# Kernel tuning notes

Hardware: AMD Instinct MI355X
Metric: run time of the kernel (lower is better)

## Reference

```python
import jax, jax.numpy as jnp
import numpy as np

N_NODES = 50000
N_EDGES = 500000
N_RELS = 460
D = 128
N_LAYERS = 2
RRELU_SLOPE = (1.0 / 8.0 + 1.0 / 3.0) / 2.0  # F.rrelu eval-mode negative slope


def setup_inputs() -> dict:
    key = jax.random.key(0)
    ks = jax.random.split(key, 9)
    return {
        "node_feats": jax.random.normal(ks[0], (N_NODES, D), dtype=jnp.float32),
        "rel_emb": jax.random.normal(ks[1], (N_RELS, D), dtype=jnp.float32),
        "norm": jax.random.uniform(ks[2], (N_NODES, 1), dtype=jnp.float32),
        "edge_src": jax.random.randint(ks[3], (N_EDGES,), 0, N_NODES, dtype=jnp.int32),
        "edge_dst": jax.random.randint(ks[4], (N_EDGES,), 0, N_NODES, dtype=jnp.int32),
        "edge_rel": jax.random.randint(ks[5], (N_EDGES,), 0, N_RELS, dtype=jnp.int32),
        "W_neigh": jax.random.normal(ks[6], (N_LAYERS, D, D), dtype=jnp.float32) * 0.05,
        "W_loop": jax.random.normal(ks[7], (N_LAYERS, D, D), dtype=jnp.float32) * 0.05,
        "W_evolve": jax.random.normal(ks[8], (N_LAYERS, D, D), dtype=jnp.float32) * 0.05,
    }


def reference(node_feats, rel_emb, norm, edge_src, edge_dst, edge_rel,
              W_neigh, W_loop, W_evolve):
    """RGCNCell with 2 UnionRGCNLayers (eval mode, dropout off)."""
    n = node_feats.shape[0]
    # nodes with in-degree > 0 use loop_weight, others evolve_loop_weight
    indeg = jax.ops.segment_sum(jnp.ones_like(edge_dst, dtype=node_feats.dtype),
                                edge_dst, num_segments=n)
    has_in = (indeg > 0)[:, None]  # [N,1]

    h = node_feats
    for l in range(W_neigh.shape[0]):
        # self-loop message: choose weight per node by in-degree mask
        loop_msg = jnp.where(has_in, h @ W_loop[l], h @ W_evolve[l])  # [N,D]
        # message: gather src h + relation emb, transform  (gather-GEMM)
        msg = (h[edge_src] + rel_emb[edge_rel]) @ W_neigh[l]  # [E,D]
        # scatter-sum to dst, then apply per-node norm (apply_func)
        agg = jax.ops.segment_sum(msg, edge_dst, num_segments=n) * norm  # [N,D]
        h = agg + loop_msg
        # F.rrelu in eval mode == leaky relu with slope (lower+upper)/2
        h = jnp.where(h >= 0, h, RRELU_SLOPE * h)
    return h
```

## Files before the change

### kernel.cpp

```cpp
#include <hip/hip_runtime.h>

#define DD 128
#define CAP 64
static constexpr float SLOPE = (1.0f/8.0f + 1.0f/3.0f) * 0.5f;

typedef __attribute__((ext_vector_type(8))) short bf16x8;
typedef __attribute__((ext_vector_type(4))) float f32x4;

__device__ inline unsigned short f2bf(float x) {
    unsigned u = __builtin_bit_cast(unsigned, x);
    unsigned r = (u + 0x7FFFu + ((u >> 16) & 1u)) >> 16;
    return (unsigned short)r;
}
__device__ inline float bflo(unsigned u) {
    unsigned v = u << 16; return __builtin_bit_cast(float, v);
}
__device__ inline float bfhi(unsigned u) {
    unsigned v = u & 0xFFFF0000u; return __builtin_bit_cast(float, v);
}
__device__ inline float2 bf2f2(unsigned u) {
    return make_float2(bflo(u), bfhi(u));
}

__global__ __launch_bounds__(256) void init_k(
    const float* __restrict__ Wn, const float* __restrict__ Wl,
    const float* __restrict__ node, const float* __restrict__ rel_emb,
    unsigned short* __restrict__ Wt, int* __restrict__ slots,
    unsigned short* __restrict__ hbf, int N, int R, int NB)
{
    int b = blockIdx.x;
    if (b < 64) {
        int i = b * 256 + threadIdx.x;
        int l = i >> 13;
        int rem = i & 8191;
        int n = rem >> 5;
        int k0 = (rem & 31) * 4;
        const float* src = (n < 128) ? (Wn + l * DD * DD + n)
                                     : (Wl + l * DD * DD + (n - 128));
        unsigned short o0 = f2bf(src[(k0 + 0) * DD]);
        unsigned short o1 = f2bf(src[(k0 + 1) * DD]);
        unsigned short o2 = f2bf(src[(k0 + 2) * DD]);
        unsigned short o3 = f2bf(src[(k0 + 3) * DD]);
        *(ushort4*)&Wt[((size_t)l * 256 + n) * DD + k0] = make_ushort4(o0, o1, o2, o3);
    } else if (b < 64 + NB) {
        int i = (b - 64) * 256 + threadIdx.x;
        if (i < N) slots[i] = 0;
    } else {
        long c = (long)(b - 64 - NB) * 256 + threadIdx.x;
        long total = (long)(N + R) * 16;
        if (c >= total) return;
        long r = c >> 4;
        int  ch = (int)(c & 15);
        const float* s = (r < N) ? (node + r * DD + ch * 8)
                                 : (rel_emb + (r - N) * DD + ch * 8);
        float4 v0 = *(const float4*)s;
        float4 v1 = *(const float4*)(s + 4);
        union { bf16x8 v; unsigned short u[8]; } t;
        t.u[0] = f2bf(v0.x); t.u[1] = f2bf(v0.y);
        t.u[2] = f2bf(v0.z); t.u[3] = f2bf(v0.w);
        t.u[4] = f2bf(v1.x); t.u[5] = f2bf(v1.y);
        t.u[6] = f2bf(v1.z); t.u[7] = f2bf(v1.w);
        *(bf16x8*)&hbf[r * DD + ch * 8] = t.v;
    }
}

__global__ __launch_bounds__(256) void fill_k(const int* __restrict__ esrc,
                                              const int* __restrict__ edst,
                                              const int* __restrict__ erel,
                                              int* __restrict__ slots,
                                              int* __restrict__ spack, int E) {
    int e = blockIdx.x * 256 + threadIdx.x;
    if (e >= E) return;
    int d = edst[e];
    int slot = atomicAdd(&slots[d], 1);
    if (slot < CAP) spack[(size_t)d * CAP + slot] = esrc[e] | (erel[e] << 17);
}

__global__ __launch_bounds__(512) void gemm_dual_mfma_k(
    const unsigned short* __restrict__ Abf,
    const unsigned short* __restrict__ Wt,
    unsigned short* __restrict__ hWn,
    unsigned short* __restrict__ loopm,
    unsigned short* __restrict__ rW,
    int N, int M)
{
    __shared__ unsigned short Wsm[256 * DD];
    int tid = threadIdx.x;
    int w = tid >> 6, lane = tid & 63;
    int wm = w >> 2, wn = w & 3;
    int g = lane >> 4, q = lane & 15;
    int row0 = blockIdx.x * 128 + wm * 64;

    bf16x8 a[4][4];
    #pragma unroll
    for (int s = 0; s < 4; ++s)
        #pragma unroll
        for (int mi = 0; mi < 4; ++mi) {
            int r = row0 + mi * 16 + q;
            if (r >= M) r = M - 1;
            a[s][mi] = *(const bf16x8*)&Abf[(size_t)r * DD + s * 32 + g * 8];
        }

    #pragma unroll
    for (int it = 0; it < 8; ++it) {
        int ci = it * 512 + tid;
        uint4 wv = *(const uint4*)((const char*)Wt + (size_t)ci * 16);
        int lin = ci * 16;
        int row = lin >> 8;
        int off = lin ^ ((row & 7) << 4);
        *(uint4*)((char*)Wsm + off) = wv;
    }
    __syncthreads();

    int sw = (q & 7) << 4;
    f32x4 acc[4][4];
    #pragma unroll
    for (int mi = 0; mi < 4; ++mi)
        #pragma unroll
        for (int ni = 0; ni < 4; ++ni)
            acc[mi][ni] = (f32x4){0.f, 0.f, 0.f, 0.f};

    #pragma unroll
    for (int s = 0; s < 4; ++s) {
        int off = 64 * s + 16 * g;
        bf16x8 b[4];
        #pragma unroll
        for (int ni = 0; ni < 4; ++ni) {
            int n = wn * 64 + ni * 16 + q;
            b[ni] = *(const bf16x8*)((const char*)Wsm + n * 256 + (off ^ sw));
        }
        #pragma unroll
        for (int mi = 0; mi < 4; ++mi)
            #pragma unroll
            for (int ni = 0; ni < 4; ++ni)
                acc[mi][ni] = __builtin_amdgcn_mfma_f32_16x16x32_bf16(
                    a[s][mi], b[ni], acc[mi][ni], 0, 0, 0);
    }
    __syncthreads();

    char* Cb = (char*)Wsm;
    #pragma unroll
    for (int mi = 0; mi < 4; ++mi)
        #pragma unroll
        for (int ni = 0; ni < 4; ++ni) {
            int col = wn * 64 + ni * 16 + q;
            #pragma unroll
            for (int j = 0; j < 4; ++j) {
                int row = wm * 64 + mi * 16 + g * 4 + j;
                int off = row * 512 + ((col * 2) ^ (((row >> 2) & 7) << 5));
                *(unsigned short*)(Cb + off) = f2bf(acc[mi][ni][j]);
            }
        }
    __syncthreads();

    int brow0 = blockIdx.x * 128;
    #pragma unroll
    for (int c0 = 0; c0 < 8; ++c0) {
        int c = c0 * 512 + tid;
        int row = c >> 5, colc = c & 31;
        int off = row * 512 + ((colc * 16) ^ (((row >> 2) & 7) << 5));
        bf16x8 v = *(const bf16x8*)(Cb + off);
        int grow = brow0 + row;
        int col = colc * 8;
        if (grow < N) {
            if (col < DD) *(bf16x8*)&hWn[(size_t)grow * DD + col] = v;
            else          *(bf16x8*)&loopm[(size_t)grow * DD + col - DD] = v;
        } else if (grow < M && col < DD) {
            *(bf16x8*)&rW[(size_t)(grow - N) * DD + col] = v;
        }
    }
}

#define ACC8(A, B) do { \
    acc0 += bf2f2((A).x) + bf2f2((B).x); \
    acc1 += bf2f2((A).y) + bf2f2((B).y); \
    acc2 += bf2f2((A).z) + bf2f2((B).z); \
    acc3 += bf2f2((A).w) + bf2f2((B).w); \
} while (0)

template<bool LAYER1>
__global__ __launch_bounds__(256) void aggregate_k(
    const unsigned short* __restrict__ hWn, const unsigned short* __restrict__ rW,
    const int* __restrict__ spack,
    const int* __restrict__ counts,
    const unsigned short* __restrict__ loopm, const float* __restrict__ norm,
    const unsigned short* __restrict__ hbf,
    const float* __restrict__ We,
    unsigned short* __restrict__ hbf_out,
    float* __restrict__ fout,
    int N)
{
    int t = blockIdx.x * 256 + threadIdx.x;
    int r = t >> 5;
    if (r >= N) return;
    int eg = (t >> 4) & 1;
    int sl = t & 15;
    int cnt = counts[r];
    size_t boff = (size_t)sl * 16;

    float nv = norm[r];
    uint4 lu = *(const uint4*)((const char*)loopm + (size_t)r * 256 + boff);

    float2 acc0 = make_float2(0.f, 0.f), acc1 = acc0, acc2 = acc0, acc3 = acc0;

    if (cnt == 0) {
        for (int k = eg * 64; k < eg * 64 + 64; ++k) {
            float hk = bflo((unsigned)hbf[(size_t)r * DD + k]);
            const float* wr = We + (size_t)k * DD + sl * 8;
            float4 w0 = *(const float4*)wr;
            float4 w1 = *(const float4*)(wr + 4);
            acc0.x += hk * w0.x; acc0.y += hk * w0.y;
            acc1.x += hk * w0.z; acc1.y += hk * w0.w;
            acc2.x += hk * w1.x; acc2.y += hk * w1.y;
            acc3.x += hk * w1.z; acc3.y += hk * w1.w;
        }
    } else {
        const char* hb = (const char*)hWn;
        const char* rb = (const char*)rW;
        int beg = r * CAP;
        int end = beg + cnt;
        int i = beg + eg;
        for (; i + 2 < end; i += 4) {
            int p0 = spack[i], p1 = spack[i + 2];
            uint4 a0 = *(const uint4*)(hb + (size_t)(p0 & 0x1FFFF) * 256 + boff);
            uint4 b0 = *(const uint4*)(rb + (size_t)(p0 >> 17) * 256 + boff);
            uint4 a1 = *(const uint4*)(hb + (size_t)(p1 & 0x1FFFF) * 256 + boff);
            uint4 b1 = *(const uint4*)(rb + (size_t)(p1 >> 17) * 256 + boff);
            ACC8(a0, b0); ACC8(a1, b1);
        }
        if (i < end) {
            int p0 = spack[i];
            uint4 a0 = *(const uint4*)(hb + (size_t)(p0 & 0x1FFFF) * 256 + boff);
            uint4 b0 = *(const uint4*)(rb + (size_t)(p0 >> 17) * 256 + boff);
            ACC8(a0, b0);
        }
    }

    acc0.x += __shfl_xor(acc0.x, 16); acc0.y += __shfl_xor(acc0.y, 16);
    acc1.x += __shfl_xor(acc1.x, 16); acc1.y += __shfl_xor(acc1.y, 16);
    acc2.x += __shfl_xor(acc2.x, 16); acc2.y += __shfl_xor(acc2.y, 16);
    acc3.x += __shfl_xor(acc3.x, 16); acc3.y += __shfl_xor(acc3.y, 16);

    if (eg != 0) return;

    float o[8];
    if (cnt == 0) {
        o[0] = acc0.x; o[1] = acc0.y; o[2] = acc1.x; o[3] = acc1.y;
        o[4] = acc2.x; o[5] = acc2.y; o[6] = acc3.x; o[7] = acc3.y;
    } else {
        o[0] = acc0.x * nv + bflo(lu.x);
        o[1] = acc0.y * nv + bfhi(lu.x);
        o[2] = acc1.x * nv + bflo(lu.y);
        o[3] = acc1.y * nv + bfhi(lu.y);
        o[4] = acc2.x * nv + bflo(lu.z);
        o[5] = acc2.y * nv + bfhi(lu.z);
        o[6] = acc3.x * nv + bflo(lu.w);
        o[7] = acc3.y * nv + bfhi(lu.w);
    }

    #pragma unroll
    for (int j = 0; j < 8; ++j) o[j] = o[j] >= 0.f ? o[j] : SLOPE * o[j];

    if constexpr (LAYER1) {
        union { bf16x8 v; unsigned short u[8]; } t2;
        #pragma unroll
        for (int j = 0; j < 8; ++j) t2.u[j] = f2bf(o[j]);
        *(bf16x8*)&hbf_out[(size_t)r * DD + sl * 8] = t2.v;
    } else {
        float* op = &fout[(size_t)r * DD + sl * 8];
        *(float4*)op       = make_float4(o[0], o[1], o[2], o[3]);
        *(float4*)(op + 4) = make_float4(o[4], o[5], o[6], o[7]);
    }
}

extern "C" void kernel_launch(void* const* d_in, const int* in_sizes, int n_in,
                              void* d_out, int out_size, void* d_ws, size_t ws_size,
                              hipStream_t stream) {
    const float* node    = (const float*)d_in[0];
    const float* rel_emb = (const float*)d_in[1];
    const float* norm    = (const float*)d_in[2];
    const int*   esrc    = (const int*)d_in[3];
    const int*   edst    = (const int*)d_in[4];
    const int*   erel    = (const int*)d_in[5];
    const float* Wn      = (const float*)d_in[6];
    const float* Wl      = (const float*)d_in[7];
    const float* We      = (const float*)d_in[8];
    int N = in_sizes[0] / DD;
    int R = in_sizes[1] / DD;
    int E = in_sizes[3];
    float* out = (float*)d_out;

    char* w = (char*)d_ws;
    auto alloc = [&](size_t bytes) {
        void* p = (void*)w;
        w += (bytes + 255) & ~(size_t)255;
        return p;
    };
    int*            slots  = (int*)           alloc((size_t)N * 4);
    int*            spack  = (int*)           alloc((size_t)N * CAP * 4);
    unsigned short* Wt     = (unsigned short*)alloc((size_t)2 * 256 * DD * 2);
    unsigned short* rW     = (unsigned short*)alloc((size_t)R * DD * 2);
    unsigned short* hWn    = (unsigned short*)alloc((size_t)N * DD * 2);
    unsigned short* loopm  = (unsigned short*)alloc((size_t)N * DD * 2);
    unsigned short* hbf    = (unsigned short*)alloc((size_t)(N + R) * DD * 2);

    int NB = (N + 255) / 256;
    int CB = (int)(((long)(N + R) * 16 + 255) / 256);
    int M = N + R;

    init_k<<<64 + NB + CB, 256, 0, stream>>>(Wn, Wl, node, rel_emb,
                                             Wt, slots, hbf, N, R, NB);
    fill_k<<<(E + 255) / 256, 256, 0, stream>>>(esrc, edst, erel, slots, spack, E);

    int gemm_blocks = (M + 127) / 128;
    int agg_blocks  = (N * 32 + 255) / 256;

    gemm_dual_mfma_k<<<gemm_blocks, 512, 0, stream>>>(
        hbf, Wt, hWn, loopm, rW, N, M);
    aggregate_k<true><<<agg_blocks, 256, 0, stream>>>(
        hWn, rW, spack, slots, loopm, norm, hbf, We, hbf, nullptr, N);

    gemm_dual_mfma_k<<<gemm_blocks, 512, 0, stream>>>(
        hbf, Wt + (size_t)256 * DD, hWn, loopm, rW, N, M);
    aggregate_k<false><<<agg_blocks, 256, 0, stream>>>(
        hWn, rW, spack, slots, loopm, norm, hbf,
        We + (size_t)DD * DD, nullptr, out, N);
}
```

Measured before the change: 126.3 us.

## Stage relation embeddings in shared memory with persistent aggregate blocks

The aggregate kernel becomes a persistent grid of 256 blocks with 1024 threads each. Each block first copies the transformed relation table rW (up to 512 relations × 128 bf16, 128KB) into LDS, then loops over 32-node chunks. Relation rows are read from LDS instead of global memory. The trade-offs are a per-block preload cost, reduced occupancy (one 1024-thread block per CU because of the large LDS footprint), and no bounds guard if R exceeds RMAX.

```diff
diff --git a/kernel.cpp b/kernel.cpp
--- a/kernel.cpp
+++ b/kernel.cpp
@@ -2,6 +2,7 @@
 
 #define DD 128
 #define CAP 64
+#define RMAX 512
 static constexpr float SLOPE = (1.0f/8.0f + 1.0f/3.0f) * 0.5f;
 
 typedef __attribute__((ext_vector_type(8))) short bf16x8;
@@ -179,7 +180,7 @@
 } while (0)
 
 template<bool LAYER1>
-__global__ __launch_bounds__(256) void aggregate_k(
+__global__ __launch_bounds__(1024, 1) void aggregate_k(
     const unsigned short* __restrict__ hWn, const unsigned short* __restrict__ rW,
     const int* __restrict__ spack,
     const int* __restrict__ counts,
@@ -188,88 +189,105 @@
     const float* __restrict__ We,
     unsigned short* __restrict__ hbf_out,
     float* __restrict__ fout,
-    int N)
+    int N, int R)
 {
-    int t = blockIdx.x * 256 + threadIdx.x;
-    int r = t >> 5;
-    if (r >= N) return;
-    int eg = (t >> 4) & 1;
-    int sl = t & 15;
-    int cnt = counts[r];
+    __shared__ unsigned short rWs[RMAX * DD];
+    int tid = threadIdx.x;
+
+    int nck = R * 16;
+    #pragma unroll
+    for (int it = 0; it < 8; ++it) {
+        int ci = it * 1024 + tid;
+        if (ci < nck)
+            *(uint4*)((char*)rWs + (size_t)ci * 16) =
+                *(const uint4*)((const char*)rW + (size_t)ci * 16);
+    }
+    __syncthreads();
+
+    int eg = (tid >> 4) & 1;
+    int sl = tid & 15;
     size_t boff = (size_t)sl * 16;
-
-    float nv = norm[r];
-    uint4 lu = *(const uint4*)((const char*)loopm + (size_t)r * 256 + boff);
-
-    float2 acc0 = make_float2(0.f, 0.f), acc1 = acc0, acc2 = acc0, acc3 = acc0;
-
-    if (cnt == 0) {
-        for (int k = eg * 64; k < eg * 64 + 64; ++k) {
-            float hk = bflo((unsigned)hbf[(size_t)r * DD + k]);
-            const float* wr = We + (size_t)k * DD + sl * 8;
-            float4 w0 = *(const float4*)wr;
-            float4 w1 = *(const float4*)(wr + 4);
-            acc0.x += hk * w0.x; acc0.y += hk * w0.y;
-            acc1.x += hk * w0.z; acc1.y += hk * w0.w;
-            acc2.x += hk * w1.x; acc2.y += hk * w1.y;
-            acc3.x += hk * w1.z; acc3.y += hk * w1.w;
-        }
-    } else {
-        const char* hb = (const char*)hWn;
-        const char* rb = (const char*)rW;
-        int beg = r * CAP;
-        int end = beg + cnt;
-        int i = beg + eg;
-        for (; i + 2 < end; i += 4) {
-            int p0 = spack[i], p1 = spack[i + 2];
-            uint4 a0 = *(const uint4*)(hb + (size_t)(p0 & 0x1FFFF) * 256 + boff);
-            uint4 b0 = *(const uint4*)(rb + (size_t)(p0 >> 17) * 256 + boff);
-            uint4 a1 = *(const uint4*)(hb + (size_t)(p1 & 0x1FFFF) * 256 + boff);
-            uint4 b1 = *(const uint4*)(rb + (size_t)(p1 >> 17) * 256 + boff);
-            ACC8(a0, b0); ACC8(a1, b1);
-        }
-        if (i < end) {
-            int p0 = spack[i];
-            uint4 a0 = *(const uint4*)(hb + (size_t)(p0 & 0x1FFFF) * 256 + boff);
-            uint4 b0 = *(const uint4*)(rb + (size_t)(p0 >> 17) * 256 + boff);
-            ACC8(a0, b0);
-        }
-    }
-
-    acc0.x += __shfl_xor(acc0.x, 16); acc0.y += __shfl_xor(acc0.y, 16);
-    acc1.x += __shfl_xor(acc1.x, 16); acc1.y += __shfl_xor(acc1.y, 16);
-    acc2.x += __shfl_xor(acc2.x, 16); acc2.y += __shfl_xor(acc2.y, 16);
-    acc3.x += __shfl_xor(acc3.x, 16); acc3.y += __shfl_xor(acc3.y, 16);
-
-    if (eg != 0) return;
-
-    float o[8];
-    if (cnt == 0) {
-        o[0] = acc0.x; o[1] = acc0.y; o[2] = acc1.x; o[3] = acc1.y;
-        o[4] = acc2.x; o[5] = acc2.y; o[6] = acc3.x; o[7] = acc3.y;
-    } else {
-        o[0] = acc0.x * nv + bflo(lu.x);
-        o[1] = acc0.y * nv + bfhi(lu.x);
-        o[2] = acc1.x * nv + bflo(lu.y);
-        o[3] = acc1.y * nv + bfhi(lu.y);
-        o[4] = acc2.x * nv + bflo(lu.z);
-        o[5] = acc2.y * nv + bfhi(lu.z);
-        o[6] = acc3.x * nv + bflo(lu.w);
-        o[7] = acc3.y * nv + bfhi(lu.w);
-    }
-
-    #pragma unroll
-    for (int j = 0; j < 8; ++j) o[j] = o[j] >= 0.f ? o[j] : SLOPE * o[j];
-
-    if constexpr (LAYER1) {
-        union { bf16x8 v; unsigned short u[8]; } t2;
-        #pragma unroll
-        for (int j = 0; j < 8; ++j) t2.u[j] = f2bf(o[j]);
-        *(bf16x8*)&hbf_out[(size_t)r * DD + sl * 8] = t2.v;
-    } else {
-        float* op = &fout[(size_t)r * DD + sl * 8];
-        *(float4*)op       = make_float4(o[0], o[1], o[2], o[3]);
-        *(float4*)(op + 4) = make_float4(o[4], o[5], o[6], o[7]);
+    int rloc = tid >> 5;
+    int nch = (N + 31) >> 5;
+
+    for (int ch = blockIdx.x; ch < nch; ch += gridDim.x) {
+        int r = ch * 32 + rloc;
+        if (r >= N) continue;
+        int cnt = counts[r];
+
+        float nv = norm[r];
+        uint4 lu = *(const uint4*)((const char*)loopm + (size_t)r * 256 + boff);
+
+        float2 acc0 = make_float2(0.f, 0.f), acc1 = acc0, acc2 = acc0, acc3 = acc0;
+
+        if (cnt == 0) {
+            for (int k = eg * 64; k < eg * 64 + 64; ++k) {
+                float hk = bflo((unsigned)hbf[(size_t)r * DD + k]);
+                const float* wr = We + (size_t)k * DD + sl * 8;
+                float4 w0 = *(const float4*)wr;
+                float4 w1 = *(const float4*)(wr + 4);
+                acc0.x += hk * w0.x; acc0.y += hk * w0.y;
+                acc1.x += hk * w0.z; acc1.y += hk * w0.w;
+                acc2.x += hk * w1.x; acc2.y += hk * w1.y;
+                acc3.x += hk * w1.z; acc3.y += hk * w1.w;
+            }
+        } else {
+            const char* hb = (const char*)hWn;
+            const char* rls = (const char*)rWs;
+            int beg = r * CAP;
+            int end = beg + cnt;
+            int i = beg + eg;
+            for (; i + 2 < end; i += 4) {
+                int p0 = spack[i], p1 = spack[i + 2];
+                uint4 a0 = *(const uint4*)(hb + (size_t)(p0 & 0x1FFFF) * 256 + boff);
+                uint4 b0 = *(const uint4*)(rls + (size_t)(p0 >> 17) * 256 + boff);
+                uint4 a1 = *(const uint4*)(hb + (size_t)(p1 & 0x1FFFF) * 256 + boff);
+                uint4 b1 = *(const uint4*)(rls + (size_t)(p1 >> 17) * 256 + boff);
+                ACC8(a0, b0); ACC8(a1, b1);
+            }
+            if (i < end) {
+                int p0 = spack[i];
+                uint4 a0 = *(const uint4*)(hb + (size_t)(p0 & 0x1FFFF) * 256 + boff);
+                uint4 b0 = *(const uint4*)(rls + (size_t)(p0 >> 17) * 256 + boff);
+                ACC8(a0, b0);
+            }
+        }
+
+        acc0.x += __shfl_xor(acc0.x, 16); acc0.y += __shfl_xor(acc0.y, 16);
+        acc1.x += __shfl_xor(acc1.x, 16); acc1.y += __shfl_xor(acc1.y, 16);
+        acc2.x += __shfl_xor(acc2.x, 16); acc2.y += __shfl_xor(acc2.y, 16);
+        acc3.x += __shfl_xor(acc3.x, 16); acc3.y += __shfl_xor(acc3.y, 16);
+
+        if (eg != 0) continue;
+
+        float o[8];
+        if (cnt == 0) {
+            o[0] = acc0.x; o[1] = acc0.y; o[2] = acc1.x; o[3] = acc1.y;
+            o[4] = acc2.x; o[5] = acc2.y; o[6] = acc3.x; o[7] = acc3.y;
+        } else {
+            o[0] = acc0.x * nv + bflo(lu.x);
+            o[1] = acc0.y * nv + bfhi(lu.x);
+            o[2] = acc1.x * nv + bflo(lu.y);
+            o[3] = acc1.y * nv + bfhi(lu.y);
+            o[4] = acc2.x * nv + bflo(lu.z);
+            o[5] = acc2.y * nv + bfhi(lu.z);
+            o[6] = acc3.x * nv + bflo(lu.w);
+            o[7] = acc3.y * nv + bfhi(lu.w);
+        }
+
+        #pragma unroll
+        for (int j = 0; j < 8; ++j) o[j] = o[j] >= 0.f ? o[j] : SLOPE * o[j];
+
+        if constexpr (LAYER1) {
+            union { bf16x8 v; unsigned short u[8]; } t2;
+            #pragma unroll
+            for (int j = 0; j < 8; ++j) t2.u[j] = f2bf(o[j]);
+            *(bf16x8*)&hbf_out[(size_t)r * DD + sl * 8] = t2.v;
+        } else {
+            float* op = &fout[(size_t)r * DD + sl * 8];
+            *(float4*)op       = make_float4(o[0], o[1], o[2], o[3]);
+            *(float4*)(op + 4) = make_float4(o[4], o[5], o[6], o[7]);
+        }
     }
 }
 
@@ -313,16 +331,16 @@
     fill_k<<<(E + 255) / 256, 256, 0, stream>>>(esrc, edst, erel, slots, spack, E);
 
     int gemm_blocks = (M + 127) / 128;
-    int agg_blocks  = (N * 32 + 255) / 256;
+    int agg_blocks  = 256;
 
     gemm_dual_mfma_k<<<gemm_blocks, 512, 0, stream>>>(
         hbf, Wt, hWn, loopm, rW, N, M);
-    aggregate_k<true><<<agg_blocks, 256, 0, stream>>>(
-        hWn, rW, spack, slots, loopm, norm, hbf, We, hbf, nullptr, N);
+    aggregate_k<true><<<agg_blocks, 1024, 0, stream>>>(
+        hWn, rW, spack, slots, loopm, norm, hbf, We, hbf, nullptr, N, R);
 
     gemm_dual_mfma_k<<<gemm_blocks, 512, 0, stream>>>(
         hbf, Wt + (size_t)256 * DD, hWn, loopm, rW, N, M);
-    aggregate_k<false><<<agg_blocks, 256, 0, stream>>>(
+    aggregate_k<false><<<agg_blocks, 1024, 0, stream>>>(
         hWn, rW, spack, slots, loopm, norm, hbf,
-        We + (size_t)DD * DD, nullptr, out, N);
-}
+        We + (size_t)DD * DD, nullptr, out, N, R);
+}
```

New measurement: 143.9 us. 13.9% more time.
